# Optimization experiments

Hardware: AMD Instinct MI355X
Metric: run time of the kernel (lower is better)

Reference implementation:

```python
import jax, jax.numpy as jnp
import numpy as np

NUM_NODES = 100000
NUM_EDGES = 640000
IN_DIM = 128
OUT_DIM = 128
NUM_REL = 16


def setup_inputs() -> dict:
    key = jax.random.key(0)
    k1, k2, k3, k4, k5 = jax.random.split(key, 5)
    x = jax.random.normal(k1, (NUM_NODES, IN_DIM), dtype=jnp.float32)
    edge_index = jax.random.randint(k2, (2, NUM_EDGES), 0, NUM_NODES, dtype=jnp.int64)
    edge_types = jax.random.randint(k3, (NUM_EDGES,), 0, NUM_REL, dtype=jnp.int64)
    # xavier-uniform-ish params
    rw_bound = float(np.sqrt(6.0 / (IN_DIM * OUT_DIM + NUM_REL)))
    relation_weights = jax.random.uniform(k4, (NUM_REL, IN_DIM, OUT_DIM), dtype=jnp.float32, minval=-rw_bound, maxval=rw_bound)
    sw_bound = float(np.sqrt(6.0 / (IN_DIM + OUT_DIM)))
    self_weight = jax.random.uniform(k5, (IN_DIM, OUT_DIM), dtype=jnp.float32, minval=-sw_bound, maxval=sw_bound)
    bias = jnp.zeros((OUT_DIM,), dtype=jnp.float32)
    return {
        'x': x,
        'edge_index': edge_index,
        'edge_types': edge_types,
        'relation_weights': relation_weights,
        'self_weight': self_weight,
        'bias': bias,
    }


def reference(x, edge_index, edge_types, relation_weights, self_weight, bias):
    num_nodes = x.shape[0]
    # self loop transform: (N, out)
    self_msg = x @ self_weight
    # transform all nodes by every relation weight once: (R, N, out)
    transformed = jnp.einsum('ni,rio->rno', x, relation_weights)
    src = edge_index[0]
    dst = edge_index[1]
    # per-edge message: pick (relation, source) transformed feature -> (E, out)
    msgs = transformed[edge_types, src]
    # scatter-add into destination nodes
    neighbor_msg = jax.ops.segment_sum(msgs, dst, num_segments=num_nodes)
    # dropout=0.0 (eval) -> identity
    return jax.nn.relu(self_msg + neighbor_msg + bias)
```

## Files before the change

### kernel.cpp

```cpp
#include <hip/hip_runtime.h>

#define N_NODES 100000
#define N_EDGES 640000
#define IN_DIM  128
#define OUT_DIM 128
#define N_REL   16
#define EPB     64
#define MEPB    128
#define SELF_PAD 100096
#define MAX_SLOTS (SELF_PAD + N_EDGES + 2048)
#define SENT    (N_EDGES + N_NODES)
#define MSG_ROWS (N_EDGES + N_NODES + 128)
#define NB_SCAN ((N_NODES + 255) / 256)
#define CVT_XB  (N_NODES * IN_DIM / 4 / 256)
#define CVT_WB  (17 * 16384 / 256)
#define HIST_B  ((N_EDGES + 255) / 256)
#define SELF_B  (SELF_PAD / 256)

typedef unsigned short u16;
typedef unsigned int   u32;
typedef __attribute__((ext_vector_type(8))) short bf16x8;
typedef __attribute__((ext_vector_type(4))) float f32x4;

__device__ inline u16 f2bf(float f) {
    u32 u = __builtin_bit_cast(u32, f);
    return (u16)((u + 0x7fffu + ((u >> 16) & 1u)) >> 16);
}
__device__ inline float bf2f(u16 s) {
    u32 u = ((u32)s) << 16;
    return __builtin_bit_cast(float, u);
}

__global__ __launch_bounds__(256) void k_pre(const float* __restrict__ x,
                                             const float* __restrict__ rw,
                                             const float* __restrict__ sw,
                                             const int* __restrict__ etype,
                                             const int* __restrict__ dst,
                                             u16* __restrict__ xb,
                                             u16* __restrict__ wt,
                                             int* __restrict__ counts_rel,
                                             int* __restrict__ dst_count,
                                             int* __restrict__ sorted) {
    int b = blockIdx.x, t = threadIdx.x;
    if (b < CVT_XB) {
        int i = b * 256 + t;
        float4 v = ((const float4*)x)[i];
        ushort4 p; p.x = f2bf(v.x); p.y = f2bf(v.y); p.z = f2bf(v.z); p.w = f2bf(v.w);
        ((ushort4*)xb)[i] = p;
    } else if (b < CVT_XB + CVT_WB) {
        int i = (b - CVT_XB) * 256 + t;
        int r = i >> 14, rem = i & 16383;
        int k = rem >> 7, np = rem & 127;
        float v = (r < 16) ? rw[i] : sw[rem];
        int c = np >> 4, nn = np & 15, kk = k >> 5, q = (k >> 3) & 3, j = k & 7;
        wt[(size_t)r * 16384 + (c * 4 + kk) * 512 + (q * 16 + nn) * 8 + j] = f2bf(v);
    } else if (b < CVT_XB + CVT_WB + HIST_B) {
        __shared__ int bins[N_REL];
        if (t < N_REL) bins[t] = 0;
        __syncthreads();
        int e = (b - CVT_XB - CVT_WB) * 256 + t;
        if (e < N_EDGES) {
            atomicAdd(&bins[etype[e]], 1);
            atomicAdd(&dst_count[dst[e]], 1);
        }
        __syncthreads();
        if (t < N_REL && bins[t]) atomicAdd(&counts_rel[t], bins[t]);
    } else {
        int i = (b - CVT_XB - CVT_WB - HIST_B) * 256 + t;
        sorted[i] = (i < N_NODES) ? (N_EDGES + i) : SENT;
    }
}

__global__ __launch_bounds__(256) void k_scan1(const int* __restrict__ dst_count,
                                               int* __restrict__ row_ptr,
                                               int* __restrict__ part) {
    __shared__ int buf[2][256];
    int t = threadIdx.x;
    int i = blockIdx.x * 256 + t;
    int v = (i < N_NODES) ? (dst_count[i] + 1) : 0;
    buf[0][t] = v;
    __syncthreads();
    int cur = 0;
    #pragma unroll
    for (int off = 1; off < 256; off <<= 1) {
        int nxt = cur ^ 1;
        int s = buf[cur][t];
        if (t >= off) s += buf[cur][t - off];
        buf[nxt][t] = s;
        __syncthreads();
        cur = nxt;
    }
    int inc = buf[cur][t];
    if (i < N_NODES) row_ptr[i] = inc - v;
    if (t == 255) part[blockIdx.x] = inc;
}

__global__ __launch_bounds__(512) void k_mid2(int* __restrict__ part,
                                              const int* __restrict__ counts,
                                              int* __restrict__ cursor,
                                              int* __restrict__ seg,
                                              int* __restrict__ sorted) {
    int t = threadIdx.x;
    if (blockIdx.x == 0) {
        __shared__ int buf[2][512];
        int v = (t < NB_SCAN) ? part[t] : 0;
        buf[0][t] = v;
        __syncthreads();
        int cur = 0;
        #pragma unroll
        for (int off = 1; off < 512; off <<= 1) {
            int nxt = cur ^ 1;
            int s = buf[cur][t];
            if (t >= off) s += buf[cur][t - off];
            buf[nxt][t] = s;
            __syncthreads();
            cur = nxt;
        }
        int inc = buf[cur][t];
        if (t < NB_SCAN) part[t] = inc - v;
    } else {
        __shared__ int s_seg[N_REL + 1];
        if (t == 0) {
            int s = SELF_PAD;
            for (int r = 0; r < N_REL; ++r) {
                cursor[r] = s; seg[r] = s; s_seg[r] = s;
                s += (counts[r] + 127) & ~127;
            }
            seg[N_REL] = s; s_seg[N_REL] = s;
        }
        __syncthreads();
        for (int r = 0; r < N_REL; ++r) {
            int b = s_seg[r] + counts[r], e2 = s_seg[r + 1];
            if (b + t < e2) sorted[b + t] = SENT;
        }
        for (int i = s_seg[N_REL] + t; i < MAX_SLOTS; i += 512)
            sorted[i] = SENT;
    }
}

__global__ __launch_bounds__(256) void k_scan3(int* __restrict__ row_ptr,
                                               const int* __restrict__ part,
                                               int* __restrict__ cursor_dst) {
    int t = threadIdx.x;
    int i = blockIdx.x * 256 + t;
    if (i < N_NODES) {
        int r = row_ptr[i] + part[blockIdx.x];
        row_ptr[i] = r;
        cursor_dst[i] = r + 1;
    }
    if (i == 0) row_ptr[N_NODES] = N_EDGES + N_NODES;
}

__global__ __launch_bounds__(256) void k_scatter_rel(const int* __restrict__ etype,
                                                     int* __restrict__ cursor,
                                                     int* __restrict__ sorted) {
    __shared__ int bins[N_REL];
    __shared__ int base[N_REL];
    int t = threadIdx.x;
    if (t < N_REL) bins[t] = 0;
    __syncthreads();
    int e = blockIdx.x * 256 + t;
    int rel = 0;
    bool valid = (e < N_EDGES);
    if (valid) { rel = etype[e]; atomicAdd(&bins[rel], 1); }
    __syncthreads();
    if (t < N_REL) {
        base[t] = bins[t] ? atomicAdd(&cursor[t], bins[t]) : 0;
        bins[t] = 0;
    }
    __syncthreads();
    if (valid) {
        int p = atomicAdd(&bins[rel], 1);
        sorted[base[rel] + p] = e;
    }
}

__global__ __launch_bounds__(256, 4) void k_msg_mfma(const u16* __restrict__ xb,
                                                     const u16* __restrict__ wt,
                                                     const int* __restrict__ src,
                                                     const int* __restrict__ etype,
                                                     const int* __restrict__ dst,
                                                     const int* __restrict__ sorted,
                                                     const int* __restrict__ row_ptr,
                                                     int* __restrict__ cursor_dst,
                                                     u16* __restrict__ msgs) {
    __shared__ u16 s_w[128 * 128];
    __shared__ int s_src[MEPB], s_pos[MEPB];
    int t = threadIdx.x;
    int e0 = blockIdx.x * MEPB;

    int ee0 = sorted[e0];
    int relb = (ee0 < N_EDGES) ? etype[ee0] : N_REL;
    const uint4* wsrc = (const uint4*)(wt + (size_t)relb * 16384);
    for (int i = t; i < 2048; i += 256)
        *(uint4*)&s_w[i * 8] = wsrc[i];
    if (t < MEPB) {
        int eid = sorted[e0 + t];
        int sv, pv;
        if (eid < N_EDGES) {
            sv = src[eid];
            pv = atomicAdd(&cursor_dst[dst[eid]], 1);
        } else if (eid < SENT) {
            sv = eid - N_EDGES;
            pv = row_ptr[sv];
        } else {
            sv = 0;
            pv = SENT + ((e0 + t) & 127);
        }
        s_src[t] = sv; s_pos[t] = pv;
    }
    __syncthreads();

    int wv = t >> 6, lane = t & 63;
    int n = lane & 15, q = lane >> 4;
    int eb = wv * 32;

    bf16x8 bx[2][4];
    int p[2];
    #pragma unroll
    for (int g = 0; g < 2; ++g) {
        int en = eb + g * 16 + n;
        const u16* xrow = xb + (size_t)s_src[en] * 128 + q * 8;
        p[g] = s_pos[en];
        #pragma unroll
        for (int kk = 0; kk < 4; ++kk)
            bx[g][kk] = *(const bf16x8*)(xrow + kk * 32);
    }

    uint4 uv[2][4];
    #pragma unroll
    for (int c = 0; c < 8; ++c) {
        bf16x8 aw[4];
        #pragma unroll
        for (int kk = 0; kk < 4; ++kk)
            aw[kk] = *(const bf16x8*)&s_w[(c * 4 + kk) * 512 + lane * 8];
        #pragma unroll
        for (int g = 0; g < 2; ++g) {
            f32x4 acc = {0.f, 0.f, 0.f, 0.f};
            #pragma unroll
            for (int kk = 0; kk < 4; ++kk)
                acc = __builtin_amdgcn_mfma_f32_16x16x32_bf16(aw[kk], bx[g][kk], acc, 0, 0, 0);
            u32 lo = (u32)f2bf(acc[0]) | ((u32)f2bf(acc[1]) << 16);
            u32 hi = (u32)f2bf(acc[2]) | ((u32)f2bf(acc[3]) << 16);
            if ((c & 1) == 0) { uv[g][c >> 1].x = lo; uv[g][c >> 1].y = hi; }
            else              { uv[g][c >> 1].z = lo; uv[g][c >> 1].w = hi; }
        }
    }
    #pragma unroll
    for (int g = 0; g < 2; ++g) {
        u32* mrow = (u32*)(msgs + (size_t)p[g] * 128 + q * 32);
        #pragma unroll
        for (int j = 0; j < 4; ++j)
            *(uint4*)(mrow + j * 4) = uv[g][j];
    }
}

__global__ __launch_bounds__(256) void k_gather(const int* __restrict__ row_ptr,
                                                const u16* __restrict__ msgs,
                                                const float* __restrict__ bias,
                                                float* __restrict__ out) {
    int wid  = (blockIdx.x * 256 + threadIdx.x) >> 6;
    int lane = threadIdx.x & 63;
    if (wid >= N_NODES) return;
    int r0 = row_ptr[wid], r1 = row_ptr[wid + 1];
    int h = lane & 15, quarter = lane >> 4;
    const uint4* m = (const uint4*)msgs;
    float s[8] = {0.f,0.f,0.f,0.f,0.f,0.f,0.f,0.f};
    for (int i = r0 + quarter; i < r1; i += 4) {
        uint4 v = m[(size_t)i * 16 + h];
        s[0] += bf2f((u16)(v.x & 0xffffu)); s[1] += bf2f((u16)(v.x >> 16));
        s[2] += bf2f((u16)(v.y & 0xffffu)); s[3] += bf2f((u16)(v.y >> 16));
        s[4] += bf2f((u16)(v.z & 0xffffu)); s[5] += bf2f((u16)(v.z >> 16));
        s[6] += bf2f((u16)(v.w & 0xffffu)); s[7] += bf2f((u16)(v.w >> 16));
    }
    #pragma unroll
    for (int j = 0; j < 8; ++j) {
        s[j] += __shfl_xor(s[j], 16);
        s[j] += __shfl_xor(s[j], 32);
    }
    if (quarter == 0) {
        int c0 = (2 * h) & 7, c1 = (2 * h + 1) & 7, qq = h >> 2;
        float4 b0 = *(const float4*)&bias[c0 * 16 + qq * 4];
        float4 b1 = *(const float4*)&bias[c1 * 16 + qq * 4];
        float* ob = out + (size_t)wid * 128;
        float4 v0, v1;
        v0.x = fmaxf(s[0] + b0.x, 0.f); v0.y = fmaxf(s[1] + b0.y, 0.f);
        v0.z = fmaxf(s[2] + b0.z, 0.f); v0.w = fmaxf(s[3] + b0.w, 0.f);
        v1.x = fmaxf(s[4] + b1.x, 0.f); v1.y = fmaxf(s[5] + b1.y, 0.f);
        v1.z = fmaxf(s[6] + b1.z, 0.f); v1.w = fmaxf(s[7] + b1.w, 0.f);
        *(float4*)(ob + c0 * 16 + qq * 4) = v0;
        *(float4*)(ob + c1 * 16 + qq * 4) = v1;
    }
}

__global__ __launch_bounds__(128) void k_self_old(const float* __restrict__ x,
                                                  const float* __restrict__ sw,
                                                  const float* __restrict__ bias,
                                                  float* __restrict__ out) {
    __shared__ float s_x[8][IN_DIM];
    int t = threadIdx.x;
    int n0 = blockIdx.x * 8;
    for (int i = t; i < 8 * IN_DIM; i += 128) {
        int r = i >> 7, j = i & 127;
        s_x[r][j] = x[(size_t)(n0 + r) * IN_DIM + j];
    }
    __syncthreads();
    float acc[8] = {0.f,0.f,0.f,0.f,0.f,0.f,0.f,0.f};
    for (int k = 0; k < IN_DIM; ++k) {
        float w = sw[k * OUT_DIM + t];
        #pragma unroll
        for (int i = 0; i < 8; ++i) acc[i] += s_x[i][k] * w;
    }
    float b = bias[t];
    #pragma unroll
    for (int i = 0; i < 8; ++i)
        out[(size_t)(n0 + i) * OUT_DIM + t] = acc[i] + b;
}

__global__ __launch_bounds__(256) void k_hist_rel(const int* __restrict__ etype,
                                                  int* __restrict__ counts_rel) {
    __shared__ int bins[N_REL];
    int t = threadIdx.x;
    if (t < N_REL) bins[t] = 0;
    __syncthreads();
    int e = blockIdx.x * 256 + t;
    if (e < N_EDGES) atomicAdd(&bins[etype[e]], 1);
    __syncthreads();
    if (t < N_REL && bins[t]) atomicAdd(&counts_rel[t], bins[t]);
}

__global__ void k_scan_rel(const int* __restrict__ counts, int* __restrict__ cursor) {
    if (threadIdx.x == 0) {
        int s = 0;
        for (int r = 0; r < N_REL; ++r) { cursor[r] = s; s += counts[r]; }
    }
}

__global__ __launch_bounds__(256) void k_edge_atomic(const float* __restrict__ x,
                                              const float* __restrict__ rw,
                                              const int* __restrict__ src,
                                              const int* __restrict__ dst,
                                              const int* __restrict__ etype,
                                              const int* __restrict__ sorted,
                                              float* __restrict__ out) {
    __shared__ int s_src[EPB], s_dst[EPB], s_rel[EPB];
    __shared__ float s_x[EPB][IN_DIM];
    int t = threadIdx.x;
    int e0 = blockIdx.x * EPB;
    if (t < EPB) {
        int eid = sorted[e0 + t];
        s_src[t] = src[eid]; s_dst[t] = dst[eid]; s_rel[t] = etype[eid];
    }
    __syncthreads();
    for (int i = t; i < EPB * IN_DIM; i += 256) {
        int e = i >> 7, j = i & 127;
        s_x[e][j] = x[(size_t)s_src[e] * IN_DIM + j];
    }
    int rel0 = s_rel[0];
    bool uni = true;
    for (int i = 1; i < EPB; ++i) uni &= (s_rel[i] == rel0);
    __syncthreads();
    int cg = t & 31, eg = t >> 5;
    for (int i = 0; i < 8; ++i) {
        int e = eg * 8 + i;
        int rel = uni ? rel0 : s_rel[e];
        const float4* Wr = (const float4*)(rw + (size_t)rel * IN_DIM * OUT_DIM);
        float a0=0.f, a1=0.f, a2=0.f, a3=0.f;
        for (int k = 0; k < 128; ++k) {
            float4 w = Wr[k * 32 + cg];
            float xv = s_x[e][k];
            a0 += xv * w.x; a1 += xv * w.y; a2 += xv * w.z; a3 += xv * w.w;
        }
        float* o = out + (size_t)s_dst[e] * OUT_DIM + cg * 4;
        atomicAdd(o + 0, a0); atomicAdd(o + 1, a1);
        atomicAdd(o + 2, a2); atomicAdd(o + 3, a3);
    }
}

__global__ void k_relu(float* __restrict__ out) {
    int i = blockIdx.x * blockDim.x + threadIdx.x;
    float4* o4 = (float4*)out;
    const int n4 = N_NODES * OUT_DIM / 4;
    if (i < n4) {
        float4 v = o4[i];
        v.x = fmaxf(v.x, 0.f); v.y = fmaxf(v.y, 0.f);
        v.z = fmaxf(v.z, 0.f); v.w = fmaxf(v.w, 0.f);
        o4[i] = v;
    }
}

extern "C" void kernel_launch(void* const* d_in, const int* in_sizes, int n_in,
                              void* d_out, int out_size, void* d_ws, size_t ws_size,
                              hipStream_t stream) {
    const float* x     = (const float*)d_in[0];
    const int*   eidx  = (const int*)d_in[1];
    const int*   etype = (const int*)d_in[2];
    const float* rw    = (const float*)d_in[3];
    const float* sw    = (const float*)d_in[4];
    const float* bias  = (const float*)d_in[5];
    float* out = (float*)d_out;
    const int* src = eidx;
    const int* dst = eidx + N_EDGES;

    int* counts_rel = (int*)d_ws;
    int* cursor_rel = counts_rel + 16;
    int* seg        = cursor_rel + 16;
    int* part       = seg + 32;
    int* dst_count  = part + 512;
    int* row_ptr    = dst_count + N_NODES;
    int* cursor_dst = row_ptr + N_NODES + 1;
    int* sorted     = cursor_dst + N_NODES;
    size_t off = (((char*)(sorted + MAX_SLOTS) - (char*)d_ws) + 255) & ~(size_t)255;
    u16* xb   = (u16*)((char*)d_ws + off);
    u16* wtb  = xb + (size_t)N_NODES * 128;
    u16* msgs = wtb + 17 * 16384;
    size_t need = (size_t)((char*)(msgs + (size_t)MSG_ROWS * 128) - (char*)d_ws);

    const int MB = MAX_SLOTS / MEPB;

    if (ws_size >= need) {
        hipMemsetAsync(d_ws, 0, (size_t)(576 + N_NODES) * sizeof(int), stream);
        k_pre<<<CVT_XB + CVT_WB + HIST_B + SELF_B, 256, 0, stream>>>(
            x, rw, sw, etype, dst, xb, wtb, counts_rel, dst_count, sorted);
        k_scan1<<<NB_SCAN, 256, 0, stream>>>(dst_count, row_ptr, part);
        k_mid2<<<2, 512, 0, stream>>>(part, counts_rel, cursor_rel, seg, sorted);
        k_scan3<<<NB_SCAN, 256, 0, stream>>>(row_ptr, part, cursor_dst);
        k_scatter_rel<<<HIST_B, 256, 0, stream>>>(etype, cursor_rel, sorted);

        k_msg_mfma<<<MB, 256, 0, stream>>>(xb, wtb, src, etype, dst, sorted,
                                           row_ptr, cursor_dst, msgs);
        k_gather<<<(N_NODES * 64 + 255) / 256, 256, 0, stream>>>(row_ptr, msgs, bias, out);
    } else {
        hipMemsetAsync(counts_rel, 0, 16 * sizeof(int), stream);
        k_hist_rel<<<HIST_B, 256, 0, stream>>>(etype, counts_rel);
        k_scan_rel<<<1, 64, 0, stream>>>(counts_rel, cursor_rel);
        k_scatter_rel<<<HIST_B, 256, 0, stream>>>(etype, cursor_rel, sorted);
        k_self_old<<<N_NODES / 8, 128, 0, stream>>>(x, sw, bias, out);
        k_edge_atomic<<<N_EDGES / EPB, 256, 0, stream>>>(x, rw, src, dst, etype, sorted, out);
        k_relu<<<(N_NODES * OUT_DIM / 4 + 255) / 256, 256, 0, stream>>>(out);
    }
}
```

Baseline: 327.4 us.

## Fuse message transform and destination aggregation into per-node-block MFMA kernel

```diff
diff --git a/kernel.cpp b/kernel.cpp
--- a/kernel.cpp
+++ b/kernel.cpp
@@ -6,19 +6,19 @@
 #define OUT_DIM 128
 #define N_REL   16
 #define EPB     64
-#define MEPB    128
-#define SELF_PAD 100096
-#define MAX_SLOTS (SELF_PAD + N_EDGES + 2048)
-#define SENT    (N_EDGES + N_NODES)
-#define MSG_ROWS (N_EDGES + N_NODES + 128)
 #define NB_SCAN ((N_NODES + 255) / 256)
 #define CVT_XB  (N_NODES * IN_DIM / 4 / 256)
 #define CVT_WB  (17 * 16384 / 256)
 #define HIST_B  ((N_EDGES + 255) / 256)
-#define SELF_B  (SELF_PAD / 256)
+#define FNB     64
+#define FCAP    1024
+#define FB      ((N_NODES + FNB - 1) / FNB)
+#define N_SLOTS (N_EDGES + N_NODES)
+#define SCAT_B  ((N_SLOTS + 255) / 256)
 
 typedef unsigned short u16;
 typedef unsigned int   u32;
+typedef unsigned long long u64;
 typedef __attribute__((ext_vector_type(8))) short bf16x8;
 typedef __attribute__((ext_vector_type(4))) float f32x4;
 
@@ -34,13 +34,10 @@
 __global__ __launch_bounds__(256) void k_pre(const float* __restrict__ x,
                                              const float* __restrict__ rw,
                                              const float* __restrict__ sw,
-                                             const int* __restrict__ etype,
                                              const int* __restrict__ dst,
                                              u16* __restrict__ xb,
                                              u16* __restrict__ wt,
-                                             int* __restrict__ counts_rel,
-                                             int* __restrict__ dst_count,
-                                             int* __restrict__ sorted) {
+                                             int* __restrict__ dst_count) {
     int b = blockIdx.x, t = threadIdx.x;
     if (b < CVT_XB) {
         int i = b * 256 + t;
@@ -54,20 +51,9 @@
         float v = (r < 16) ? rw[i] : sw[rem];
         int c = np >> 4, nn = np & 15, kk = k >> 5, q = (k >> 3) & 3, j = k & 7;
         wt[(size_t)r * 16384 + (c * 4 + kk) * 512 + (q * 16 + nn) * 8 + j] = f2bf(v);
-    } else if (b < CVT_XB + CVT_WB + HIST_B) {
-        __shared__ int bins[N_REL];
-        if (t < N_REL) bins[t] = 0;
-        __syncthreads();
+    } else {
         int e = (b - CVT_XB - CVT_WB) * 256 + t;
-        if (e < N_EDGES) {
-            atomicAdd(&bins[etype[e]], 1);
-            atomicAdd(&dst_count[dst[e]], 1);
-        }
-        __syncthreads();
-        if (t < N_REL && bins[t]) atomicAdd(&counts_rel[t], bins[t]);
-    } else {
-        int i = (b - CVT_XB - CVT_WB - HIST_B) * 256 + t;
-        sorted[i] = (i < N_NODES) ? (N_EDGES + i) : SENT;
+        if (e < N_EDGES) atomicAdd(&dst_count[dst[e]], 1);
     }
 }
 
@@ -95,47 +81,24 @@
     if (t == 255) part[blockIdx.x] = inc;
 }
 
-__global__ __launch_bounds__(512) void k_mid2(int* __restrict__ part,
-                                              const int* __restrict__ counts,
-                                              int* __restrict__ cursor,
-                                              int* __restrict__ seg,
-                                              int* __restrict__ sorted) {
-    int t = threadIdx.x;
-    if (blockIdx.x == 0) {
-        __shared__ int buf[2][512];
-        int v = (t < NB_SCAN) ? part[t] : 0;
-        buf[0][t] = v;
-        __syncthreads();
-        int cur = 0;
-        #pragma unroll
-        for (int off = 1; off < 512; off <<= 1) {
-            int nxt = cur ^ 1;
-            int s = buf[cur][t];
-            if (t >= off) s += buf[cur][t - off];
-            buf[nxt][t] = s;
-            __syncthreads();
-            cur = nxt;
-        }
-        int inc = buf[cur][t];
-        if (t < NB_SCAN) part[t] = inc - v;
-    } else {
-        __shared__ int s_seg[N_REL + 1];
-        if (t == 0) {
-            int s = SELF_PAD;
-            for (int r = 0; r < N_REL; ++r) {
-                cursor[r] = s; seg[r] = s; s_seg[r] = s;
-                s += (counts[r] + 127) & ~127;
-            }
-            seg[N_REL] = s; s_seg[N_REL] = s;
-        }
-        __syncthreads();
-        for (int r = 0; r < N_REL; ++r) {
-            int b = s_seg[r] + counts[r], e2 = s_seg[r + 1];
-            if (b + t < e2) sorted[b + t] = SENT;
-        }
-        for (int i = s_seg[N_REL] + t; i < MAX_SLOTS; i += 512)
-            sorted[i] = SENT;
-    }
+__global__ __launch_bounds__(512) void k_part(int* __restrict__ part) {
+    __shared__ int buf[2][512];
+    int t = threadIdx.x;
+    int v = (t < NB_SCAN) ? part[t] : 0;
+    buf[0][t] = v;
+    __syncthreads();
+    int cur = 0;
+    #pragma unroll
+    for (int off = 1; off < 512; off <<= 1) {
+        int nxt = cur ^ 1;
+        int s = buf[cur][t];
+        if (t >= off) s += buf[cur][t - off];
+        buf[nxt][t] = s;
+        __syncthreads();
+        cur = nxt;
+    }
+    int inc = buf[cur][t];
+    if (t < NB_SCAN) part[t] = inc - v;
 }
 
 __global__ __launch_bounds__(256) void k_scan3(int* __restrict__ row_ptr,
@@ -148,7 +111,180 @@
         row_ptr[i] = r;
         cursor_dst[i] = r + 1;
     }
-    if (i == 0) row_ptr[N_NODES] = N_EDGES + N_NODES;
+    if (i == 0) row_ptr[N_NODES] = N_SLOTS;
+}
+
+__global__ __launch_bounds__(256) void k_scatter_dst(const int* __restrict__ src,
+                                                     const int* __restrict__ dst,
+                                                     const int* __restrict__ etype,
+                                                     const int* __restrict__ row_ptr,
+                                                     int* __restrict__ cursor_dst,
+                                                     u64* __restrict__ pk) {
+    int i = blockIdx.x * 256 + threadIdx.x;
+    if (i < N_EDGES) {
+        int d = dst[i];
+        int p = atomicAdd(&cursor_dst[d], 1);
+        pk[p] = (u64)(u32)src[i] | ((u64)(u32)etype[i] << 20) | ((u64)(u32)d << 32);
+    } else if (i < N_SLOTS) {
+        int nn = i - N_EDGES;
+        pk[row_ptr[nn]] = (u64)(u32)nn | ((u64)16u << 20) | ((u64)(u32)nn << 32);
+    }
+}
+
+__global__ __launch_bounds__(512, 8) void k_fused(const u16* __restrict__ xb,
+                                                  const u16* __restrict__ wt,
+                                                  const u64* __restrict__ pk,
+                                                  const int* __restrict__ row_ptr,
+                                                  const float* __restrict__ bias,
+                                                  float* __restrict__ out) {
+    __shared__ float s_acc[FNB * 128];
+    __shared__ u32   s_ord[FCAP];
+    __shared__ int   s_bins[32];
+    __shared__ int   s_off[18];
+    __shared__ int   s_cur[18];
+    __shared__ u32   s_grp[64];
+    __shared__ int   s_ngrp;
+    __shared__ float s_bias[128];
+
+    int t = threadIdx.x;
+    int n0 = blockIdx.x * FNB;
+    int nend = min(n0 + FNB, N_NODES);
+    int sb = row_ptr[n0], se = row_ptr[nend];
+
+    #pragma unroll
+    for (int i = t; i < FNB * 128 / 4; i += 512)
+        ((float4*)s_acc)[i] = make_float4(0.f, 0.f, 0.f, 0.f);
+    if (t < 128) s_bias[t] = bias[t];
+
+    int wv = t >> 6, lane = t & 63;
+    int n = lane & 15, q = lane >> 4;
+
+    for (int c0 = sb; c0 < se; c0 += FCAP) {
+        int cnt = min(FCAP, se - c0);
+        if (t < 32) s_bins[t] = 0;
+        __syncthreads();
+        u64 my0 = 0, my1 = 0;
+        if (t < cnt)       { my0 = pk[c0 + t];       atomicAdd(&s_bins[(int)((my0 >> 20) & 31)], 1); }
+        if (t + 512 < cnt) { my1 = pk[c0 + t + 512]; atomicAdd(&s_bins[(int)((my1 >> 20) & 31)], 1); }
+        __syncthreads();
+        if (t == 0) {
+            int s = 0, ng = 0;
+            for (int r = 0; r < 17; ++r) {
+                s_off[r] = s; s_cur[r] = s;
+                int c = s_bins[r];
+                for (int k = 0; k < c; k += 32) s_grp[ng++] = (u32)((r << 12) | (s + k));
+                s += c;
+            }
+            s_off[17] = s; s_ngrp = ng;
+        }
+        __syncthreads();
+        if (t < cnt) {
+            int r = (int)((my0 >> 20) & 31);
+            int p = atomicAdd(&s_cur[r], 1);
+            s_ord[p] = (u32)(my0 & 0xFFFFFu) | ((((u32)(my0 >> 32)) - (u32)n0) << 20);
+        }
+        if (t + 512 < cnt) {
+            int r = (int)((my1 >> 20) & 31);
+            int p = atomicAdd(&s_cur[r], 1);
+            s_ord[p] = (u32)(my1 & 0xFFFFFu) | ((((u32)(my1 >> 32)) - (u32)n0) << 20);
+        }
+        __syncthreads();
+        int ng = s_ngrp;
+        for (int g = wv; g < ng; g += 8) {
+            u32 gr = s_grp[g];
+            int r = gr >> 12, st = gr & 0xFFF;
+            int gend = s_off[r + 1]; if (st + 32 < gend) gend = st + 32;
+            const u16* wr = wt + (size_t)r * 16384;
+            bf16x8 bx[2][4]; int dl[2]; bool val[2];
+            #pragma unroll
+            for (int gg = 0; gg < 2; ++gg) {
+                int en = st + gg * 16 + n;
+                bool v = (en < gend);
+                u32 o = v ? s_ord[en] : 0u;
+                val[gg] = v; dl[gg] = (int)(o >> 20);
+                const u16* xrow = xb + (size_t)(o & 0xFFFFFu) * 128 + q * 8;
+                #pragma unroll
+                for (int kk = 0; kk < 4; ++kk)
+                    bx[gg][kk] = *(const bf16x8*)(xrow + kk * 32);
+            }
+            #pragma unroll
+            for (int c = 0; c < 8; ++c) {
+                bf16x8 aw[4];
+                #pragma unroll
+                for (int kk = 0; kk < 4; ++kk)
+                    aw[kk] = *(const bf16x8*)(wr + (c * 4 + kk) * 512 + lane * 8);
+                #pragma unroll
+                for (int gg = 0; gg < 2; ++gg) {
+                    f32x4 acc = {0.f, 0.f, 0.f, 0.f};
+                    #pragma unroll
+                    for (int kk = 0; kk < 4; ++kk)
+                        acc = __builtin_amdgcn_mfma_f32_16x16x32_bf16(aw[kk], bx[gg][kk], acc, 0, 0, 0);
+                    if (val[gg]) {
+                        float* ap = s_acc + dl[gg] * 128;
+                        int xsw = dl[gg] & 31;
+                        #pragma unroll
+                        for (int j = 0; j < 4; ++j)
+                            atomicAdd(&ap[(c * 16 + q * 4 + j) ^ xsw], acc[j]);
+                    }
+                }
+            }
+        }
+        __syncthreads();
+    }
+    int rows = nend - n0;
+    for (int i = t; i < rows * 32; i += 512) {
+        int nn = i >> 5, c4 = (i & 31) * 4;
+        int xsw = nn & 31;
+        float4 v;
+        v.x = fmaxf(s_acc[nn * 128 + ((c4 + 0) ^ xsw)] + s_bias[c4 + 0], 0.f);
+        v.y = fmaxf(s_acc[nn * 128 + ((c4 + 1) ^ xsw)] + s_bias[c4 + 1], 0.f);
+        v.z = fmaxf(s_acc[nn * 128 + ((c4 + 2) ^ xsw)] + s_bias[c4 + 2], 0.f);
+        v.w = fmaxf(s_acc[nn * 128 + ((c4 + 3) ^ xsw)] + s_bias[c4 + 3], 0.f);
+        *(float4*)(out + (size_t)(n0 + nn) * 128 + c4) = v;
+    }
+}
+
+__global__ __launch_bounds__(128) void k_self_old(const float* __restrict__ x,
+                                                  const float* __restrict__ sw,
+                                                  const float* __restrict__ bias,
+                                                  float* __restrict__ out) {
+    __shared__ float s_x[8][IN_DIM];
+    int t = threadIdx.x;
+    int n0 = blockIdx.x * 8;
+    for (int i = t; i < 8 * IN_DIM; i += 128) {
+        int r = i >> 7, j = i & 127;
+        s_x[r][j] = x[(size_t)(n0 + r) * IN_DIM + j];
+    }
+    __syncthreads();
+    float acc[8] = {0.f,0.f,0.f,0.f,0.f,0.f,0.f,0.f};
+    for (int k = 0; k < IN_DIM; ++k) {
+        float w = sw[k * OUT_DIM + t];
+        #pragma unroll
+        for (int i = 0; i < 8; ++i) acc[i] += s_x[i][k] * w;
+    }
+    float b = bias[t];
+    #pragma unroll
+    for (int i = 0; i < 8; ++i)
+        out[(size_t)(n0 + i) * OUT_DIM + t] = acc[i] + b;
+}
+
+__global__ __launch_bounds__(256) void k_hist_rel(const int* __restrict__ etype,
+                                                  int* __restrict__ counts_rel) {
+    __shared__ int bins[N_REL];
+    int t = threadIdx.x;
+    if (t < N_REL) bins[t] = 0;
+    __syncthreads();
+    int e = blockIdx.x * 256 + t;
+    if (e < N_EDGES) atomicAdd(&bins[etype[e]], 1);
+    __syncthreads();
+    if (t < N_REL && bins[t]) atomicAdd(&counts_rel[t], bins[t]);
+}
+
+__global__ void k_scan_rel(const int* __restrict__ counts, int* __restrict__ cursor) {
+    if (threadIdx.x == 0) {
+        int s = 0;
+        for (int r = 0; r < N_REL; ++r) { cursor[r] = s; s += counts[r]; }
+    }
 }
 
 __global__ __launch_bounds__(256) void k_scatter_rel(const int* __restrict__ etype,
@@ -172,167 +308,6 @@
     if (valid) {
         int p = atomicAdd(&bins[rel], 1);
         sorted[base[rel] + p] = e;
-    }
-}
-
-__global__ __launch_bounds__(256, 4) void k_msg_mfma(const u16* __restrict__ xb,
-                                                     const u16* __restrict__ wt,
-                                                     const int* __restrict__ src,
-                                                     const int* __restrict__ etype,
-                                                     const int* __restrict__ dst,
-                                                     const int* __restrict__ sorted,
-                                                     const int* __restrict__ row_ptr,
-                                                     int* __restrict__ cursor_dst,
-                                                     u16* __restrict__ msgs) {
-    __shared__ u16 s_w[128 * 128];
-    __shared__ int s_src[MEPB], s_pos[MEPB];
-    int t = threadIdx.x;
-    int e0 = blockIdx.x * MEPB;
-
-    int ee0 = sorted[e0];
-    int relb = (ee0 < N_EDGES) ? etype[ee0] : N_REL;
-    const uint4* wsrc = (const uint4*)(wt + (size_t)relb * 16384);
-    for (int i = t; i < 2048; i += 256)
-        *(uint4*)&s_w[i * 8] = wsrc[i];
-    if (t < MEPB) {
-        int eid = sorted[e0 + t];
-        int sv, pv;
-        if (eid < N_EDGES) {
-            sv = src[eid];
-            pv = atomicAdd(&cursor_dst[dst[eid]], 1);
-        } else if (eid < SENT) {
-            sv = eid - N_EDGES;
-            pv = row_ptr[sv];
-        } else {
-            sv = 0;
-            pv = SENT + ((e0 + t) & 127);
-        }
-        s_src[t] = sv; s_pos[t] = pv;
-    }
-    __syncthreads();
-
-    int wv = t >> 6, lane = t & 63;
-    int n = lane & 15, q = lane >> 4;
-    int eb = wv * 32;
-
-    bf16x8 bx[2][4];
-    int p[2];
-    #pragma unroll
-    for (int g = 0; g < 2; ++g) {
-        int en = eb + g * 16 + n;
-        const u16* xrow = xb + (size_t)s_src[en] * 128 + q * 8;
-        p[g] = s_pos[en];
-        #pragma unroll
-        for (int kk = 0; kk < 4; ++kk)
-            bx[g][kk] = *(const bf16x8*)(xrow + kk * 32);
-    }
-
-    uint4 uv[2][4];
-    #pragma unroll
-    for (int c = 0; c < 8; ++c) {
-        bf16x8 aw[4];
-        #pragma unroll
-        for (int kk = 0; kk < 4; ++kk)
-            aw[kk] = *(const bf16x8*)&s_w[(c * 4 + kk) * 512 + lane * 8];
-        #pragma unroll
-        for (int g = 0; g < 2; ++g) {
-            f32x4 acc = {0.f, 0.f, 0.f, 0.f};
-            #pragma unroll
-            for (int kk = 0; kk < 4; ++kk)
-                acc = __builtin_amdgcn_mfma_f32_16x16x32_bf16(aw[kk], bx[g][kk], acc, 0, 0, 0);
-            u32 lo = (u32)f2bf(acc[0]) | ((u32)f2bf(acc[1]) << 16);
-            u32 hi = (u32)f2bf(acc[2]) | ((u32)f2bf(acc[3]) << 16);
-            if ((c & 1) == 0) { uv[g][c >> 1].x = lo; uv[g][c >> 1].y = hi; }
-            else              { uv[g][c >> 1].z = lo; uv[g][c >> 1].w = hi; }
-        }
-    }
-    #pragma unroll
-    for (int g = 0; g < 2; ++g) {
-        u32* mrow = (u32*)(msgs + (size_t)p[g] * 128 + q * 32);
-        #pragma unroll
-        for (int j = 0; j < 4; ++j)
-            *(uint4*)(mrow + j * 4) = uv[g][j];
-    }
-}
-
-__global__ __launch_bounds__(256) void k_gather(const int* __restrict__ row_ptr,
-                                                const u16* __restrict__ msgs,
-                                                const float* __restrict__ bias,
-                                                float* __restrict__ out) {
-    int wid  = (blockIdx.x * 256 + threadIdx.x) >> 6;
-    int lane = threadIdx.x & 63;
-    if (wid >= N_NODES) return;
-    int r0 = row_ptr[wid], r1 = row_ptr[wid + 1];
-    int h = lane & 15, quarter = lane >> 4;
-    const uint4* m = (const uint4*)msgs;
-    float s[8] = {0.f,0.f,0.f,0.f,0.f,0.f,0.f,0.f};
-    for (int i = r0 + quarter; i < r1; i += 4) {
-        uint4 v = m[(size_t)i * 16 + h];
-        s[0] += bf2f((u16)(v.x & 0xffffu)); s[1] += bf2f((u16)(v.x >> 16));
-        s[2] += bf2f((u16)(v.y & 0xffffu)); s[3] += bf2f((u16)(v.y >> 16));
-        s[4] += bf2f((u16)(v.z & 0xffffu)); s[5] += bf2f((u16)(v.z >> 16));
-        s[6] += bf2f((u16)(v.w & 0xffffu)); s[7] += bf2f((u16)(v.w >> 16));
-    }
-    #pragma unroll
-    for (int j = 0; j < 8; ++j) {
-        s[j] += __shfl_xor(s[j], 16);
-        s[j] += __shfl_xor(s[j], 32);
-    }
-    if (quarter == 0) {
-        int c0 = (2 * h) & 7, c1 = (2 * h + 1) & 7, qq = h >> 2;
-        float4 b0 = *(const float4*)&bias[c0 * 16 + qq * 4];
-        float4 b1 = *(const float4*)&bias[c1 * 16 + qq * 4];
-        float* ob = out + (size_t)wid * 128;
-        float4 v0, v1;
-        v0.x = fmaxf(s[0] + b0.x, 0.f); v0.y = fmaxf(s[1] + b0.y, 0.f);
-        v0.z = fmaxf(s[2] + b0.z, 0.f); v0.w = fmaxf(s[3] + b0.w, 0.f);
-        v1.x = fmaxf(s[4] + b1.x, 0.f); v1.y = fmaxf(s[5] + b1.y, 0.f);
-        v1.z = fmaxf(s[6] + b1.z, 0.f); v1.w = fmaxf(s[7] + b1.w, 0.f);
-        *(float4*)(ob + c0 * 16 + qq * 4) = v0;
-        *(float4*)(ob + c1 * 16 + qq * 4) = v1;
-    }
-}
-
-__global__ __launch_bounds__(128) void k_self_old(const float* __restrict__ x,
-                                                  const float* __restrict__ sw,
-                                                  const float* __restrict__ bias,
-                                                  float* __restrict__ out) {
-    __shared__ float s_x[8][IN_DIM];
-    int t = threadIdx.x;
-    int n0 = blockIdx.x * 8;
-    for (int i = t; i < 8 * IN_DIM; i += 128) {
-        int r = i >> 7, j = i & 127;
-        s_x[r][j] = x[(size_t)(n0 + r) * IN_DIM + j];
-    }
-    __syncthreads();
-    float acc[8] = {0.f,0.f,0.f,0.f,0.f,0.f,0.f,0.f};
-    for (int k = 0; k < IN_DIM; ++k) {
-        float w = sw[k * OUT_DIM + t];
-        #pragma unroll
-        for (int i = 0; i < 8; ++i) acc[i] += s_x[i][k] * w;
-    }
-    float b = bias[t];
-    #pragma unroll
-    for (int i = 0; i < 8; ++i)
-        out[(size_t)(n0 + i) * OUT_DIM + t] = acc[i] + b;
-}
-
-__global__ __launch_bounds__(256) void k_hist_rel(const int* __restrict__ etype,
-                                                  int* __restrict__ counts_rel) {
-    __shared__ int bins[N_REL];
-    int t = threadIdx.x;
-    if (t < N_REL) bins[t] = 0;
-    __syncthreads();
-    int e = blockIdx.x * 256 + t;
-    if (e < N_EDGES) atomicAdd(&bins[etype[e]], 1);
-    __syncthreads();
-    if (t < N_REL && bins[t]) atomicAdd(&counts_rel[t], bins[t]);
-}
-
-__global__ void k_scan_rel(const int* __restrict__ counts, int* __restrict__ cursor) {
-    if (threadIdx.x == 0) {
-        int s = 0;
-        for (int r = 0; r < N_REL; ++r) { cursor[r] = s; s += counts[r]; }
     }
 }
 
@@ -402,41 +377,36 @@
     const int* src = eidx;
     const int* dst = eidx + N_EDGES;
 
-    int* counts_rel = (int*)d_ws;
-    int* cursor_rel = counts_rel + 16;
-    int* seg        = cursor_rel + 16;
-    int* part       = seg + 32;
+    int* part       = (int*)d_ws;
     int* dst_count  = part + 512;
     int* row_ptr    = dst_count + N_NODES;
     int* cursor_dst = row_ptr + N_NODES + 1;
-    int* sorted     = cursor_dst + N_NODES;
-    size_t off = (((char*)(sorted + MAX_SLOTS) - (char*)d_ws) + 255) & ~(size_t)255;
-    u16* xb   = (u16*)((char*)d_ws + off);
+    size_t off0 = (((char*)(cursor_dst + N_NODES) - (char*)d_ws) + 255) & ~(size_t)255;
+    u64* pk   = (u64*)((char*)d_ws + off0);
+    u16* xb   = (u16*)(pk + N_SLOTS);
     u16* wtb  = xb + (size_t)N_NODES * 128;
-    u16* msgs = wtb + 17 * 16384;
-    size_t need = (size_t)((char*)(msgs + (size_t)MSG_ROWS * 128) - (char*)d_ws);
-
-    const int MB = MAX_SLOTS / MEPB;
+    size_t need = (size_t)((char*)(wtb + 17 * 16384) - (char*)d_ws);
 
     if (ws_size >= need) {
-        hipMemsetAsync(d_ws, 0, (size_t)(576 + N_NODES) * sizeof(int), stream);
-        k_pre<<<CVT_XB + CVT_WB + HIST_B + SELF_B, 256, 0, stream>>>(
-            x, rw, sw, etype, dst, xb, wtb, counts_rel, dst_count, sorted);
+        hipMemsetAsync(dst_count, 0, (size_t)N_NODES * sizeof(int), stream);
+        k_pre<<<CVT_XB + CVT_WB + HIST_B, 256, 0, stream>>>(
+            x, rw, sw, dst, xb, wtb, dst_count);
         k_scan1<<<NB_SCAN, 256, 0, stream>>>(dst_count, row_ptr, part);
-        k_mid2<<<2, 512, 0, stream>>>(part, counts_rel, cursor_rel, seg, sorted);
+        k_part<<<1, 512, 0, stream>>>(part);
         k_scan3<<<NB_SCAN, 256, 0, stream>>>(row_ptr, part, cursor_dst);
-        k_scatter_rel<<<HIST_B, 256, 0, stream>>>(etype, cursor_rel, sorted);
-
-        k_msg_mfma<<<MB, 256, 0, stream>>>(xb, wtb, src, etype, dst, sorted,
-                                           row_ptr, cursor_dst, msgs);
-        k_gather<<<(N_NODES * 64 + 255) / 256, 256, 0, stream>>>(row_ptr, msgs, bias, out);
+        k_scatter_dst<<<SCAT_B, 256, 0, stream>>>(src, dst, etype, row_ptr,
+                                                  cursor_dst, pk);
+        k_fused<<<FB, 512, 0, stream>>>(xb, wtb, pk, row_ptr, bias, out);
     } else {
+        int* counts_rel = (int*)d_ws;
+        int* cursor_rel = counts_rel + 16;
+        int* sortedf    = counts_rel + 64;
         hipMemsetAsync(counts_rel, 0, 16 * sizeof(int), stream);
         k_hist_rel<<<HIST_B, 256, 0, stream>>>(etype, counts_rel);
         k_scan_rel<<<1, 64, 0, stream>>>(counts_rel, cursor_rel);
-        k_scatter_rel<<<HIST_B, 256, 0, stream>>>(etype, cursor_rel, sorted);
+        k_scatter_rel<<<HIST_B, 256, 0, stream>>>(etype, cursor_rel, sortedf);
         k_self_old<<<N_NODES / 8, 128, 0, stream>>>(x, sw, bias, out);
-        k_edge_atomic<<<N_EDGES / EPB, 256, 0, stream>>>(x, rw, src, dst, etype, sorted, out);
+        k_edge_atomic<<<N_EDGES / EPB, 256, 0, stream>>>(x, rw, src, dst, etype, sortedf, out);
         k_relu<<<(N_NODES * OUT_DIM / 4 + 255) / 256, 256, 0, stream>>>(out);
     }
 }
```

After: 784.9 us. +139.7%, slower.
